# Optimization experiments

Measured on AMD Instinct MI355X. Metric: run time of the kernel, lower is better.

## Reference

```python
import jax, jax.numpy as jnp
import numpy as np

N = 50000      # nodes
E = 600000     # edges (avg degree 12)
D_IN = 16      # node_input_size
D = 128        # hidden_size
H = 4          # num_heads
DH = D // H
L = 4          # message_passing_num
D_FF = 512     # 4*hidden FFN expansion
D_OUT = 3      # output_size


def setup_inputs() -> dict:
    key = jax.random.key(0)
    ks = iter(jax.random.split(key, 32))
    def w(shape, fan_in):
        return jax.random.normal(next(ks), shape, jnp.float32) / np.float32(np.sqrt(fan_in))
    return {
        "features": jax.random.normal(next(ks), (N, D_IN), jnp.float32),
        "senders": jax.random.randint(next(ks), (E,), 0, N),
        "receivers": jax.random.randint(next(ks), (E,), 0, N),
        "enc_w1": w((D_IN, D), D_IN), "enc_b1": jnp.zeros((D,), jnp.float32),
        "enc_w2": w((D, D), D),       "enc_b2": jnp.zeros((D,), jnp.float32),
        "wq": w((L, D, D), D), "wk": w((L, D, D), D),
        "wv": w((L, D, D), D), "wo": w((L, D, D), D),
        "ln1_s": jnp.ones((L, D), jnp.float32), "ln1_b": jnp.zeros((L, D), jnp.float32),
        "ffn_w1": w((L, D, D_FF), D), "ffn_b1": jnp.zeros((L, D_FF), jnp.float32),
        "ffn_w2": w((L, D_FF, D), D_FF), "ffn_b2": jnp.zeros((L, D), jnp.float32),
        "ln2_s": jnp.ones((L, D), jnp.float32), "ln2_b": jnp.zeros((L, D), jnp.float32),
        "dec_w1": w((D, D_OUT), D), "dec_b1": jnp.zeros((D_OUT,), jnp.float32),
        "dec_w2": w((D_OUT, D_OUT), D_OUT), "dec_b2": jnp.zeros((D_OUT,), jnp.float32),
    }


def _ln(x, s, b):
    mu = x.mean(-1, keepdims=True)
    var = ((x - mu) ** 2).mean(-1, keepdims=True)
    return (x - mu) * jax.lax.rsqrt(var + 1e-5) * s + b


def _graph_mha(x, senders, receivers, wq, wk, wv, wo):
    # Adjacency-masked attention done sparsely over the edge list
    # (equivalent to softmax over the BCOO adjacency pattern).
    n = x.shape[0]
    q = (x @ wq).reshape(n, H, DH)
    k = (x @ wk).reshape(n, H, DH)
    v = (x @ wv).reshape(n, H, DH)
    scores = (q[receivers] * k[senders]).sum(-1) / np.float32(np.sqrt(DH))  # [E,H]
    m = jax.ops.segment_max(scores, receivers, num_segments=n)             # [N,H]
    m = jnp.where(jnp.isfinite(m), m, 0.0)
    a = jnp.exp(scores - m[receivers])                                      # [E,H]
    denom = jax.ops.segment_sum(a, receivers, num_segments=n)              # [N,H]
    msg = jax.ops.segment_sum(a[:, :, None] * v[senders], receivers, num_segments=n)  # [N,H,DH]
    out = (msg / (denom[:, :, None] + 1e-9)).reshape(n, D)
    return out @ wo


def reference(features, senders, receivers,
              enc_w1, enc_b1, enc_w2, enc_b2,
              wq, wk, wv, wo, ln1_s, ln1_b,
              ffn_w1, ffn_b1, ffn_w2, ffn_b2, ln2_s, ln2_b,
              dec_w1, dec_b1, dec_w2, dec_b2):
    # encode
    x = jnp.maximum(features @ enc_w1 + enc_b1, 0.0) @ enc_w2 + enc_b2     # [N,D]
    # process: L pre-LN sparse-attention transformer blocks
    for l in range(L):
        h = _ln(x, ln1_s[l], ln1_b[l])
        x = x + _graph_mha(h, senders, receivers, wq[l], wk[l], wv[l], wo[l])
        h = _ln(x, ln2_s[l], ln2_b[l])
        x = x + jnp.maximum(h @ ffn_w1[l] + ffn_b1[l], 0.0) @ ffn_w2[l] + ffn_b2[l]
    # decode
    return jnp.maximum(x @ dec_w1 + dec_b1, 0.0) @ dec_w2 + dec_b2         # [N,D_OUT]
```

## Files before the change

kernel.cpp:

```cpp
#include <hip/hip_runtime.h>
#include <hip/hip_bf16.h>
#include <math.h>

#define D     128
#define NHEAD 4
#define DH    32
#define DFF   512
#define DIN   16
#define MAXDEG 64
#define TN    16

typedef __attribute__((ext_vector_type(8))) short bf16x8;
typedef __attribute__((ext_vector_type(4))) float f32x4;
typedef __hip_bfloat16 bf16;

#define QSCALE_L2E 0.2550348838f

#define BMQ 128

#define WAITV(N) asm volatile("s_waitcnt vmcnt(" #N ")" ::: "memory")
#define WAITLGKM asm volatile("s_waitcnt lgkmcnt(0)" ::: "memory")
#define FENCE()  asm volatile("" ::: "memory")
#define BAR() do { FENCE(); __builtin_amdgcn_s_barrier(); FENCE(); } while (0)

__device__ __forceinline__ void gll16(const bf16* g, bf16* l) {
    __builtin_amdgcn_global_load_lds((__attribute__((address_space(1))) void*)g,
                                     (__attribute__((address_space(3))) void*)l,
                                     16, 0, 0);
}

__device__ __forceinline__ ushort bfbits(float f) {
    __hip_bfloat16 b = __float2bfloat16(f);
    return *(ushort*)&b;
}

__global__ void k_fill(const int* __restrict__ recv, const int* __restrict__ senders,
                       int* __restrict__ deg, int* __restrict__ eid, int E) {
    int e = blockIdx.x * blockDim.x + threadIdx.x;
    if (e >= E) return;
    int r = recv[e];
    int pos = atomicAdd(&deg[r], 1);
    if (pos < MAXDEG) eid[r * MAXDEG + pos] = senders[e];
}

__global__ void k_wt(const float* __restrict__ wq, const float* __restrict__ wk,
                     const float* __restrict__ wv, const float* __restrict__ wo,
                     const float* __restrict__ w1, const float* __restrict__ w2,
                     const float* __restrict__ encw2,
                     bf16* __restrict__ wqkvT, bf16* __restrict__ woT,
                     bf16* __restrict__ w1T, bf16* __restrict__ w2T,
                     bf16* __restrict__ encw2T, int* __restrict__ deg,
                     int* __restrict__ eid, int N) {
    int r = blockIdx.y;
    if (r == 25) {
        int tot = N + N * MAXDEG;
        for (int i = blockIdx.x * blockDim.x + threadIdx.x; i < tot;
             i += 256 * 256) {
            if (i < N) deg[i] = 0;
            else eid[i - N] = 0;
        }
        return;
    }
    const float* src; bf16* dst; int K, Nout;
    if (r < 12) {
        int l = r / 3, sel = r % 3;
        src = (sel == 0 ? wq : sel == 1 ? wk : wv) + (size_t)l * D * D;
        dst = wqkvT + (size_t)l * 3 * D * D + (size_t)sel * D * D;
        K = D; Nout = D;
    } else if (r < 16) {
        int l = r - 12;
        src = wo + (size_t)l * D * D; dst = woT + (size_t)l * D * D; K = D; Nout = D;
    } else if (r < 20) {
        int l = r - 16;
        src = w1 + (size_t)l * D * DFF; dst = w1T + (size_t)l * D * DFF; K = D; Nout = DFF;
    } else if (r < 24) {
        int l = r - 20;
        src = w2 + (size_t)l * DFF * D; dst = w2T + (size_t)l * DFF * D; K = DFF; Nout = D;
    } else {
        src = encw2; dst = encw2T; K = D; Nout = D;
    }
    int total = K * Nout;
    int i = blockIdx.x * blockDim.x + threadIdx.x;
    if (i >= total) return;
    int k = i / Nout, j = i % Nout;
    dst[(size_t)j * K + k] = __float2bfloat16(src[i]);
}

__device__ __forceinline__ void load_afrag(const bf16* A, int arow, int quad,
                                           int N, bf16x8* afr) {
    const bf16* ab = A + (size_t)arow * D + quad * 8;
#pragma unroll
    for (int i = 0; i < 4; i++) {
        uint4 v = make_uint4(0u, 0u, 0u, 0u);
        if (arow < N) v = *(const uint4*)(ab + i * 32);
        afr[i] = *(bf16x8*)&v;
    }
}

__device__ __forceinline__ void stage_full256(bf16* lb, const bf16* src,
                                              int wave, int lane) {
#pragma unroll
    for (int k = 0; k < 8; k++) {
        int gidx = (wave * 8 + k) * 64 + lane;
        int r = gidx >> 4, gL = gidx & 15;
        gll16(src + (size_t)r * 128 + ((gL ^ (r & 15)) * 8),
              lb + (size_t)(wave * 8 + k) * 512);
    }
}

__device__ __forceinline__ void stage_full512(bf16* lb, const bf16* src,
                                              int wave, int lane) {
#pragma unroll
    for (int k = 0; k < 4; k++) {
        int gidx = (wave * 4 + k) * 64 + lane;
        int r = gidx >> 4, gL = gidx & 15;
        gll16(src + (size_t)r * 128 + ((gL ^ (r & 15)) * 8),
              lb + (size_t)(wave * 4 + k) * 512);
    }
}

__device__ __forceinline__ void stage_q(bf16* lb, const bf16* src, int rs,
                                        int wave, int lane) {
#pragma unroll
    for (int k = 0; k < 2; k++) {
        int gidx = (wave * 2 + k) * 64 + lane;
        int r = gidx >> 2, gL = gidx & 3;
        gll16(src + (size_t)r * rs + ((gL ^ ((r >> 1) & 3)) * 8),
              lb + (size_t)(wave * 2 + k) * 512);
    }
}

__device__ __forceinline__ void mfma_tile(const bf16* Wb, const bf16x8* afr,
                                          f32x4* acc, int l16, int quad) {
#pragma unroll
    for (int i = 0; i < 4; i++)
#pragma unroll
        for (int j = 0; j < 8; j++) {
            const bf16* wp = Wb + (size_t)(j * 16 + l16) * 128
                              + (size_t)((((i * 4 + quad)) ^ l16) * 8);
            acc[j] = __builtin_amdgcn_mfma_f32_16x16x32_bf16(afr[i], *(const bf16x8*)wp,
                                                             acc[j], 0, 0, 0);
        }
}

template<int OP>
__global__ __launch_bounds__(256) void k_gemm(
        const bf16* __restrict__ A, const bf16* __restrict__ Bt,
        const float* __restrict__ bias,
        const float* __restrict__ lns, const float* __restrict__ lnb,
        float* x, bf16* outB, int N) {
    __shared__ alignas(16) bf16 Wsm[128 * 128];
    int m0 = blockIdx.x * 64;
    int t = threadIdx.x;
    int wave = t >> 6, lane = t & 63;
    int quad = lane >> 4, l16 = lane & 15;
    int wm = wave * 16;

    bf16x8 afr[4];
    load_afrag(A, m0 + wm + l16, quad, N, afr);
    FENCE();
    stage_full256(Wsm, Bt, wave, lane);
    WAITV(0); BAR();

    int rowb = m0 + wm + quad * 4;
    float xv[8][4];
    if (OP == 2) {
#pragma unroll
        for (int j = 0; j < 8; j++)
#pragma unroll
            for (int r = 0; r < 4; r++) {
                int gr = rowb + r;
                xv[j][r] = (gr < N) ? x[(size_t)gr * D + j * 16 + l16] : 0.f;
            }
    }

    f32x4 acc[8];
#pragma unroll
    for (int j = 0; j < 8; j++) acc[j] = (f32x4){0.f, 0.f, 0.f, 0.f};
    mfma_tile(Wsm, afr, acc, l16, quad);

    float bv[8];
    if (OP == 5) {
#pragma unroll
        for (int j = 0; j < 8; j++) bv[j] = bias[j * 16 + l16];
    }
#pragma unroll
    for (int j = 0; j < 8; j++) {
#pragma unroll
        for (int r = 0; r < 4; r++) {
            int gr = rowb + r;
            if (gr >= N) continue;
            float val = acc[j][r];
            if (OP == 5) val += bv[j];
            if (OP == 2) val += xv[j][r];
            acc[j][r] = val;
        }
    }
    float lsv[8], lbv[8];
#pragma unroll
    for (int j = 0; j < 8; j++) {
        lsv[j] = lns[j * 16 + l16];
        lbv[j] = lnb[j * 16 + l16];
    }
#pragma unroll
    for (int r = 0; r < 4; r++) {
        float s1 = 0.f, s2 = 0.f;
#pragma unroll
        for (int j = 0; j < 8; j++) {
            float v = acc[j][r];
            s1 += v; s2 += v * v;
        }
        s1 += __shfl_xor(s1, 1, 64);  s2 += __shfl_xor(s2, 1, 64);
        s1 += __shfl_xor(s1, 2, 64);  s2 += __shfl_xor(s2, 2, 64);
        s1 += __shfl_xor(s1, 4, 64);  s2 += __shfl_xor(s2, 4, 64);
        s1 += __shfl_xor(s1, 8, 64);  s2 += __shfl_xor(s2, 8, 64);
        float mu = s1 * (1.f / 128.f);
        float var = s2 * (1.f / 128.f) - mu * mu;
        float rinv = rsqrtf(fmaxf(var, 0.f) + 1e-5f);
        int gr = rowb + r;
        if (gr >= N) continue;
#pragma unroll
        for (int j = 0; j < 8; j++) {
            int col = j * 16 + l16;
            float v = acc[j][r];
            x[(size_t)gr * D + col] = v;
            outB[(size_t)gr * D + col] =
                __float2bfloat16((v - mu) * rinv * lsv[j] + lbv[j]);
        }
    }
}

__global__ __launch_bounds__(512, 2) void k_qkv(
        const bf16* __restrict__ hb, const bf16* __restrict__ wqkvT,
        bf16* __restrict__ qb, bf16* __restrict__ kvb, int N) {
    __shared__ alignas(16) bf16 Wbuf[2][128 * 128];
    int m0 = blockIdx.x * BMQ;
    int t = threadIdx.x;
    int wave = t >> 6, lane = t & 63;
    int quad = lane >> 4, l16 = lane & 15;
    int wm = wave * 16;

    bf16x8 afr[4];
    load_afrag(hb, m0 + wm + l16, quad, N, afr);
    FENCE();
    stage_full512(Wbuf[0], wqkvT + (size_t)D * D, wave, lane);
    FENCE();
    stage_full512(Wbuf[1], wqkvT + (size_t)2 * D * D, wave, lane);
    FENCE();

    int rowb = m0 + wm + quad * 4;
    f32x4 ak[8], acc[8];
#pragma unroll
    for (int j = 0; j < 8; j++) ak[j] = (f32x4){0.f, 0.f, 0.f, 0.f};

    WAITV(4); BAR();
    __builtin_amdgcn_s_setprio(1);
    mfma_tile(Wbuf[0], afr, ak, l16, quad);
    __builtin_amdgcn_s_setprio(0);
    BAR();
    stage_full512(Wbuf[0], wqkvT, wave, lane);
    FENCE();
#pragma unroll
    for (int j = 0; j < 8; j++) acc[j] = (f32x4){0.f, 0.f, 0.f, 0.f};
    WAITV(4); BAR();
    __builtin_amdgcn_s_setprio(1);
    mfma_tile(Wbuf[1], afr, acc, l16, quad);
    __builtin_amdgcn_s_setprio(0);

#pragma unroll
    for (int j = 0; j < 8; j++) {
        int col = j * 16 + l16;
#pragma unroll
        for (int r = 0; r < 4; r++) {
            int gr = rowb + r;
            if (gr >= N) continue;
            uint kv = (uint)bfbits(ak[j][r]) | ((uint)bfbits(acc[j][r]) << 16);
            *(uint*)&kvb[((size_t)gr * D + col) * 2] = kv;
        }
    }
    FENCE();
    if (m0 + BMQ <= N) { WAITV(32); } else { WAITV(0); }
    BAR();
#pragma unroll
    for (int j = 0; j < 8; j++) acc[j] = (f32x4){0.f, 0.f, 0.f, 0.f};
    __builtin_amdgcn_s_setprio(1);
    mfma_tile(Wbuf[0], afr, acc, l16, quad);
    __builtin_amdgcn_s_setprio(0);
#pragma unroll
    for (int j = 0; j < 8; j++) {
        int col = j * 16 + l16;
#pragma unroll
        for (int r = 0; r < 4; r++) {
            int gr = rowb + r;
            if (gr >= N) continue;
            qb[(size_t)gr * D + col] = __float2bfloat16(acc[j][r] * QSCALE_L2E);
        }
    }
}

__device__ __forceinline__ void stage_ffn_q(int ts, const bf16* w1T,
                                            const bf16* w2T, bf16* Wb3,
                                            int wave, int lane) {
    int c = ts >> 3, p = ts & 7;
    const bf16* src; int rs;
    if (p < 4) { src = w1T + (size_t)(c * 128) * 128 + p * 32;       rs = 128; }
    else       { src = w2T + (size_t)(c * 128) + (p - 4) * 32;       rs = DFF; }
    stage_q(Wb3 + (size_t)(ts % 3) * (32 * 128), src, rs, wave, lane);
}

template<int MODE>
__global__ __launch_bounds__(256) void k_ffn(
        const bf16* __restrict__ hb, const bf16* __restrict__ w1T,
        const float* __restrict__ b1,
        const bf16* __restrict__ w2T, const float* __restrict__ b2,
        const float* __restrict__ lns, const float* __restrict__ lnb,
        const float* __restrict__ dw1, const float* __restrict__ db1,
        const float* __restrict__ dw2, const float* __restrict__ db2,
        float* x, bf16* outB, float* out, int N) {
    __shared__ alignas(16) bf16 Wb3[3][32 * 128];
    __shared__ alignas(16) bf16 Hsm[64 * 128];
    int m0 = blockIdx.x * 64;
    int t = threadIdx.x;
    int wave = t >> 6, lane = t & 63;
    int quad = lane >> 4, l16 = lane & 15;
    int wm = wave * 16;
    int rowb = m0 + wm + quad * 4;

    float b1pre[4][8];
#pragma unroll
    for (int c2 = 0; c2 < 4; c2++)
#pragma unroll
        for (int j = 0; j < 8; j++) b1pre[c2][j] = b1[c2 * 128 + j * 16 + l16];

    bf16x8 afr[4];
    load_afrag(hb, m0 + wm + l16, quad, N, afr);
    FENCE();
    stage_ffn_q(0, w1T, w2T, &Wb3[0][0], wave, lane);
    FENCE();
    stage_ffn_q(1, w1T, w2T, &Wb3[0][0], wave, lane);
    FENCE();

    f32x4 acc2[8], accP[8];
#pragma unroll
    for (int j = 0; j < 8; j++) acc2[j] = (f32x4){0.f, 0.f, 0.f, 0.f};
    float xv[8][4];

    int wswz = (quad ^ ((l16 >> 1) & 3)) * 8;

#pragma unroll
    for (int s = 0; s < 32; s++) {
        BAR();
        if (s + 2 < 32) {
            stage_ffn_q(s + 2, w1T, w2T, &Wb3[0][0], wave, lane);
            FENCE();
        }
        if (s < 30) { WAITV(4); } else if (s == 30) { WAITV(2); } else { WAITV(0); }
        BAR();
        const bf16* Wb = &Wb3[0][0] + (size_t)(s % 3) * (32 * 128);
        int c = s >> 3, p = s & 7;
        if (s == 31) {
#pragma unroll
            for (int j = 0; j < 8; j++)
#pragma unroll
                for (int r = 0; r < 4; r++) {
                    int gr = rowb + r;
                    xv[j][r] = (gr < N) ? x[(size_t)gr * D + j * 16 + l16] : 0.f;
                }
        }
        if (p < 4) {
            if (p == 0) {
#pragma unroll
                for (int j = 0; j < 8; j++) accP[j] = (f32x4){0.f, 0.f, 0.f, 0.f};
            }
            __builtin_amdgcn_s_setprio(1);
#pragma unroll
            for (int j = 0; j < 8; j++) {
                const bf16* wp = Wb + (size_t)(j * 16 + l16) * 32 + wswz;
                accP[j] = __builtin_amdgcn_mfma_f32_16x16x32_bf16(
                    afr[p], *(const bf16x8*)wp, accP[j], 0, 0, 0);
            }
            __builtin_amdgcn_s_setprio(0);
            if (p == 3) {
                int rw = wm + quad * 4;
#pragma unroll
                for (int j = 0; j < 8; j++) {
                    int gb = j * 2 + (l16 >> 3), ce = l16 & 7;
#pragma unroll
                    for (int r = 0; r < 4; r++) {
                        int row = rw + r;
                        Hsm[(size_t)row * 128 + (size_t)((gb ^ (row & 15)) * 8) + ce] =
                            __float2bfloat16(fmaxf(accP[j][r] + b1pre[c][j], 0.f));
                    }
                }
                WAITLGKM;
            }
        } else {
            int kq = p - 4;
            bf16x8 af2 = *(const bf16x8*)(Hsm + (size_t)(wm + l16) * 128
                              + (size_t)(((kq * 4 + quad) ^ l16) * 8));
            __builtin_amdgcn_s_setprio(1);
#pragma unroll
            for (int j = 0; j < 8; j++) {
                const bf16* wp = Wb + (size_t)(j * 16 + l16) * 32 + wswz;
                acc2[j] = __builtin_amdgcn_mfma_f32_16x16x32_bf16(
                    af2, *(const bf16x8*)wp, acc2[j], 0, 0, 0);
            }
            __builtin_amdgcn_s_setprio(0);
        }
    }

    float bv[8];
#pragma unroll
    for (int j = 0; j < 8; j++) bv[j] = b2[j * 16 + l16];
#pragma unroll
    for (int j = 0; j < 8; j++) {
#pragma unroll
        for (int r = 0; r < 4; r++) {
            int gr = rowb + r;
            if (gr >= N) continue;
            acc2[j][r] += bv[j] + xv[j][r];
        }
    }
    if (MODE == 1) {
        float dw[8][3];
#pragma unroll
        for (int j = 0; j < 8; j++) {
            int col = j * 16 + l16;
#pragma unroll
            for (int cc3 = 0; cc3 < 3; cc3++) dw[j][cc3] = dw1[col * 3 + cc3];
        }
#pragma unroll
        for (int r = 0; r < 4; r++) {
            float s0 = 0.f, s1 = 0.f, s2 = 0.f;
#pragma unroll
            for (int j = 0; j < 8; j++) {
                float v = acc2[j][r];
                s0 += v * dw[j][0]; s1 += v * dw[j][1]; s2 += v * dw[j][2];
            }
            s0 += __shfl_xor(s0, 1, 64); s1 += __shfl_xor(s1, 1, 64); s2 += __shfl_xor(s2, 1, 64);
            s0 += __shfl_xor(s0, 2, 64); s1 += __shfl_xor(s1, 2, 64); s2 += __shfl_xor(s2, 2, 64);
            s0 += __shfl_xor(s0, 4, 64); s1 += __shfl_xor(s1, 4, 64); s2 += __shfl_xor(s2, 4, 64);
            s0 += __shfl_xor(s0, 8, 64); s1 += __shfl_xor(s1, 8, 64); s2 += __shfl_xor(s2, 8, 64);
            int gr = rowb + r;
            if (l16 == 0 && gr < N) {
                float t0 = fmaxf(s0 + db1[0], 0.f);
                float t1 = fmaxf(s1 + db1[1], 0.f);
                float t2 = fmaxf(s2 + db1[2], 0.f);
#pragma unroll
                for (int o = 0; o < 3; o++)
                    out[(size_t)gr * 3 + o] =
                        t0 * dw2[0 * 3 + o] + t1 * dw2[1 * 3 + o] + t2 * dw2[2 * 3 + o] + db2[o];
            }
        }
        return;
    }
    float lsv[8], lbv[8];
#pragma unroll
    for (int j = 0; j < 8; j++) {
        lsv[j] = lns[j * 16 + l16];
        lbv[j] = lnb[j * 16 + l16];
    }
#pragma unroll
    for (int r = 0; r < 4; r++) {
        float s1 = 0.f, s2 = 0.f;
#pragma unroll
        for (int j = 0; j < 8; j++) {
            float v = acc2[j][r];
            s1 += v; s2 += v * v;
        }
        s1 += __shfl_xor(s1, 1, 64);  s2 += __shfl_xor(s2, 1, 64);
        s1 += __shfl_xor(s1, 2, 64);  s2 += __shfl_xor(s2, 2, 64);
        s1 += __shfl_xor(s1, 4, 64);  s2 += __shfl_xor(s2, 4, 64);
        s1 += __shfl_xor(s1, 8, 64);  s2 += __shfl_xor(s2, 8, 64);
        float mu = s1 * (1.f / 128.f);
        float var = s2 * (1.f / 128.f) - mu * mu;
        float rinv = rsqrtf(fmaxf(var, 0.f) + 1e-5f);
        int gr = rowb + r;
        if (gr >= N) continue;
#pragma unroll
        for (int j = 0; j < 8; j++) {
            int col = j * 16 + l16;
            float v = acc2[j][r];
            x[(size_t)gr * D + col] = v;
            outB[(size_t)gr * D + col] = __float2bfloat16((v - mu) * rinv * lsv[j] + lbv[j]);
        }
    }
}

__global__ void k_enc1(const float* __restrict__ feat,
                       const float* __restrict__ w1, const float* __restrict__ b1,
                       bf16* __restrict__ hb, int N) {
    __shared__ float fsh[TN][DIN];
    int n0 = blockIdx.x * TN;
    int j = threadIdx.x;
    int nvalid = min(TN, N - n0);
    for (int idx = j; idx < TN * DIN; idx += 128) {
        int n = idx / DIN, i = idx % DIN;
        fsh[n][i] = (n < nvalid) ? feat[(n0 + n) * DIN + i] : 0.f;
    }
    __syncthreads();
    float bb = b1[j];
#pragma unroll
    for (int n = 0; n < TN; n++) {
        float a = bb;
#pragma unroll
        for (int i = 0; i < DIN; i++) a += fsh[n][i] * w1[i * D + j];
        if (n < nvalid) hb[(size_t)(n0 + n) * D + j] = __float2bfloat16(fmaxf(a, 0.f));
    }
}

__device__ __forceinline__ void attn_edge(uint4 w, bool v, float4 qv,
                                          float& l, float& a0, float& a1,
                                          float& a2, float& a3) {
    float k0 = __uint_as_float(w.x << 16), v0 = __uint_as_float(w.x & 0xFFFF0000u);
    float k1 = __uint_as_float(w.y << 16), v1 = __uint_as_float(w.y & 0xFFFF0000u);
    float k2 = __uint_as_float(w.z << 16), v2 = __uint_as_float(w.z & 0xFFFF0000u);
    float k3 = __uint_as_float(w.w << 16), v3 = __uint_as_float(w.w & 0xFFFF0000u);
    float p = qv.x * k0 + qv.y * k1 + qv.z * k2 + qv.w * k3;
    p += __shfl_xor(p, 1, 64);
    p += __shfl_xor(p, 2, 64);
    p += __shfl_xor(p, 4, 64);
    float e = v ? exp2f(p) : 0.f;
    l += e;
    a0 += e * v0; a1 += e * v1; a2 += e * v2; a3 += e * v3;
}

__device__ __forceinline__ float4 unpackq(uint2 qw) {
    float4 qv;
    qv.x = __uint_as_float(qw.x << 16);
    qv.y = __uint_as_float(qw.x & 0xFFFF0000u);
    qv.z = __uint_as_float(qw.y << 16);
    qv.w = __uint_as_float(qw.y & 0xFFFF0000u);
    return qv;
}

__global__ __launch_bounds__(256) void k_attn(
        const bf16* __restrict__ qb, const uint* __restrict__ kvb,
        const int* __restrict__ deg, const int* __restrict__ eid,
        bf16* __restrict__ out, int N) {
    int wave = threadIdx.x >> 6, lane = threadIdx.x & 63;
    int g = lane & 7, h = (lane >> 3) & 3, slot = lane >> 5;
    int d0 = h * 32 + g * 4;
    int rbase = blockIdx.x * 16 + wave * 4;
    if (rbase >= N) return;
    const uint* kvbase = kvb + d0;

    int ssN[8];
    {
        const int* row = eid + (size_t)rbase * MAXDEG;
#pragma unroll
        for (int u = 0; u < 8; u++) ssN[u] = row[u * 2 + slot];
    }
    int cntN = min(deg[rbase], MAXDEG);
    float4 qvN = unpackq(*(const uint2*)(qb + (size_t)rbase * D + d0));

#pragma unroll
    for (int i = 0; i < 4; i++) {
        int r = rbase + i;
        if (r >= N) return;
        int cnt = cntN; float4 qv = qvN;
        uint4 w[8];
#pragma unroll
        for (int u = 0; u < 8; u++)
            w[u] = *(const uint4*)(kvbase + (size_t)ssN[u] * D);
        int rn = r + 1;
        if (i < 3 && rn < N) {
            const int* rowN = eid + (size_t)rn * MAXDEG;
#pragma unroll
            for (int u = 0; u < 8; u++) ssN[u] = rowN[u * 2 + slot];
            cntN = min(deg[rn], MAXDEG);
            qvN = unpackq(*(const uint2*)(qb + (size_t)rn * D + d0));
        }
        float l = 0.f, a0 = 0.f, a1 = 0.f, a2 = 0.f, a3 = 0.f;
#pragma unroll
        for (int u = 0; u < 8; u++)
            attn_edge(w[u], (u * 2 + slot) < cnt, qv, l, a0, a1, a2, a3);
        for (int base = 16; base < cnt; base += 16) {
            const int* row = eid + (size_t)r * MAXDEG;
            int ss[8]; bool vv[8];
#pragma unroll
            for (int u = 0; u < 8; u++) {
                int e = base + u * 2 + slot;
                vv[u] = e < cnt;
                ss[u] = row[e];
            }
            uint4 w2_[8];
#pragma unroll
            for (int u = 0; u < 8; u++)
                w2_[u] = *(const uint4*)(kvbase + (size_t)ss[u] * D);
#pragma unroll
            for (int u = 0; u < 8; u++)
                attn_edge(w2_[u], vv[u], qv, l, a0, a1, a2, a3);
        }
        l  += __shfl_xor(l, 32, 64);
        a0 += __shfl_xor(a0, 32, 64);
        a1 += __shfl_xor(a1, 32, 64);
        a2 += __shfl_xor(a2, 32, 64);
        a3 += __shfl_xor(a3, 32, 64);
        if (lane < 32) {
            float inv = 1.f / (l + 1e-9f);
            bf16 o[4];
            o[0] = __float2bfloat16(a0 * inv);
            o[1] = __float2bfloat16(a1 * inv);
            o[2] = __float2bfloat16(a2 * inv);
            o[3] = __float2bfloat16(a3 * inv);
            *(uint2*)(out + (size_t)r * D + d0) = *(uint2*)o;
        }
    }
}

extern "C" void kernel_launch(void* const* d_in, const int* in_sizes, int n_in,
                              void* d_out, int out_size, void* d_ws, size_t ws_size,
                              hipStream_t stream) {
    const float* feat    = (const float*)d_in[0];
    const int*   senders = (const int*)d_in[1];
    const int*   recv    = (const int*)d_in[2];
    const float* enc_w1  = (const float*)d_in[3];
    const float* enc_b1  = (const float*)d_in[4];
    const float* enc_w2  = (const float*)d_in[5];
    const float* enc_b2  = (const float*)d_in[6];
    const float* wq      = (const float*)d_in[7];
    const float* wk      = (const float*)d_in[8];
    const float* wv      = (const float*)d_in[9];
    const float* wo      = (const float*)d_in[10];
    const float* ln1_s   = (const float*)d_in[11];
    const float* ln1_b   = (const float*)d_in[12];
    const float* ffn_w1  = (const float*)d_in[13];
    const float* ffn_b1  = (const float*)d_in[14];
    const float* ffn_w2  = (const float*)d_in[15];
    const float* ffn_b2  = (const float*)d_in[16];
    const float* ln2_s   = (const float*)d_in[17];
    const float* ln2_b   = (const float*)d_in[18];
    const float* dec_w1  = (const float*)d_in[19];
    const float* dec_b1  = (const float*)d_in[20];
    const float* dec_w2  = (const float*)d_in[21];
    const float* dec_b2  = (const float*)d_in[22];

    int N = in_sizes[0] / DIN;
    int E = in_sizes[1];

    char* p = (char*)d_ws;
    float* x   = (float*)p;  p += (size_t)N * D * 4;
    bf16*  qb  = (bf16*)p;   p += (size_t)N * D * 2;
    bf16*  kvb = (bf16*)p;   p += (size_t)N * D * 2 * 2;
    bf16*  hb  = (bf16*)p;   p += (size_t)N * D * 2;
    int* deg   = (int*)p;    p += (size_t)N * 4;
    int* eid   = (int*)p;    p += (size_t)N * MAXDEG * 4;
    bf16* wqkvT  = (bf16*)p; p += (size_t)4 * 3 * D * D * 2;
    bf16* woT    = (bf16*)p; p += (size_t)4 * D * D * 2;
    bf16* w1T    = (bf16*)p; p += (size_t)4 * D * DFF * 2;
    bf16* w2T    = (bf16*)p; p += (size_t)4 * DFF * D * 2;
    bf16* encw2T = (bf16*)p; p += (size_t)D * D * 2;

    int gm64 = (N + 63) / 64;
    int gmQ  = (N + BMQ - 1) / BMQ;

    k_wt<<<dim3(256, 26), 256, 0, stream>>>(wq, wk, wv, wo, ffn_w1, ffn_w2, enc_w2,
                                            wqkvT, woT, w1T, w2T, encw2T, deg, eid, N);
    k_fill<<<(E + 255) / 256, 256, 0, stream>>>(recv, senders, deg, eid, E);
    k_enc1<<<(N + TN - 1) / TN, 128, 0, stream>>>(feat, enc_w1, enc_b1, hb, N);
    k_gemm<5><<<gm64, 256, 0, stream>>>(hb, encw2T, enc_b2, ln1_s, ln1_b, x, hb, N);

    for (int l = 0; l < 4; l++) {
        k_qkv<<<gmQ, 512, 0, stream>>>(hb, wqkvT + (size_t)l * 3 * D * D, qb, kvb, N);
        k_attn<<<(N + 15) / 16, 256, 0, stream>>>(qb, (const uint*)kvb, deg, eid, hb, N);
        k_gemm<2><<<gm64, 256, 0, stream>>>(hb, woT + (size_t)l * D * D,
                                            nullptr, ln2_s + l * D, ln2_b + l * D,
                                            x, hb, N);
        if (l < 3)
            k_ffn<0><<<gm64, 256, 0, stream>>>(hb, w1T + (size_t)l * D * DFF,
                                               ffn_b1 + l * DFF,
                                               w2T + (size_t)l * DFF * D, ffn_b2 + l * D,
                                               ln1_s + (l + 1) * D, ln1_b + (l + 1) * D,
                                               nullptr, nullptr, nullptr, nullptr,
                                               x, hb, nullptr, N);
        else
            k_ffn<1><<<gm64, 256, 0, stream>>>(hb, w1T + (size_t)l * D * DFF,
                                               ffn_b1 + l * DFF,
                                               w2T + (size_t)l * DFF * D, ffn_b2 + l * D,
                                               nullptr, nullptr,
                                               dec_w1, dec_b1, dec_w2, dec_b2,
                                               x, nullptr, (float*)d_out, N);
    }
}
```

Before: 644.3 us.

## Drop eid zero-fill and simplify attention to one row per wave

The setup kernel no longer zeroes the N×MAXDEG neighbour table and clears only the degree array. The attention kernel now guards neighbour-index loads with the edge count, so the stale table entries are never read. The attention kernel also goes from four rows per wave, with software prefetch of the next row's indices and query, to one row per wave with a uniform loop. This removes a large memset (about 12.8 MB) at the cost of losing cross-row prefetch overlap in attention, and launches four times as many blocks.

```diff
diff --git a/kernel.cpp b/kernel.cpp
--- a/kernel.cpp
+++ b/kernel.cpp
@@ -16,7 +16,7 @@
 
 #define QSCALE_L2E 0.2550348838f
 
-#define BMQ 128
+#define BM 128
 
 #define WAITV(N) asm volatile("s_waitcnt vmcnt(" #N ")" ::: "memory")
 #define WAITLGKM asm volatile("s_waitcnt lgkmcnt(0)" ::: "memory")
@@ -49,16 +49,11 @@
                      const float* __restrict__ encw2,
                      bf16* __restrict__ wqkvT, bf16* __restrict__ woT,
                      bf16* __restrict__ w1T, bf16* __restrict__ w2T,
-                     bf16* __restrict__ encw2T, int* __restrict__ deg,
-                     int* __restrict__ eid, int N) {
+                     bf16* __restrict__ encw2T, int* __restrict__ deg, int N) {
     int r = blockIdx.y;
     if (r == 25) {
-        int tot = N + N * MAXDEG;
-        for (int i = blockIdx.x * blockDim.x + threadIdx.x; i < tot;
-             i += 256 * 256) {
-            if (i < N) deg[i] = 0;
-            else eid[i - N] = 0;
-        }
+        int i = blockIdx.x * blockDim.x + threadIdx.x;
+        if (i < N) deg[i] = 0;
         return;
     }
     const float* src; bf16* dst; int K, Nout;
@@ -234,7 +229,7 @@
         const bf16* __restrict__ hb, const bf16* __restrict__ wqkvT,
         bf16* __restrict__ qb, bf16* __restrict__ kvb, int N) {
     __shared__ alignas(16) bf16 Wbuf[2][128 * 128];
-    int m0 = blockIdx.x * BMQ;
+    int m0 = blockIdx.x * BM;
     int t = threadIdx.x;
     int wave = t >> 6, lane = t & 63;
     int quad = lane >> 4, l16 = lane & 15;
@@ -279,7 +274,7 @@
         }
     }
     FENCE();
-    if (m0 + BMQ <= N) { WAITV(32); } else { WAITV(0); }
+    if (m0 + BM <= N) { WAITV(32); } else { WAITV(0); }
     BAR();
 #pragma unroll
     for (int j = 0; j < 8; j++) acc[j] = (f32x4){0.f, 0.f, 0.f, 0.f};
@@ -525,87 +520,57 @@
     a0 += e * v0; a1 += e * v1; a2 += e * v2; a3 += e * v3;
 }
 
-__device__ __forceinline__ float4 unpackq(uint2 qw) {
+__global__ __launch_bounds__(256) void k_attn(
+        const bf16* __restrict__ qb, const uint* __restrict__ kvb,
+        const int* __restrict__ deg, const int* __restrict__ eid,
+        bf16* __restrict__ out, int N) {
+    int wave = threadIdx.x >> 6, lane = threadIdx.x & 63;
+    int r = blockIdx.x * 4 + wave;
+    if (r >= N) return;
+    int g = lane & 7;
+    int h = (lane >> 3) & 3;
+    int slot = lane >> 5;
+    int d0 = h * 32 + g * 4;
+    uint2 qw = *(const uint2*)(qb + (size_t)r * D + d0);
     float4 qv;
     qv.x = __uint_as_float(qw.x << 16);
     qv.y = __uint_as_float(qw.x & 0xFFFF0000u);
     qv.z = __uint_as_float(qw.y << 16);
     qv.w = __uint_as_float(qw.y & 0xFFFF0000u);
-    return qv;
-}
-
-__global__ __launch_bounds__(256) void k_attn(
-        const bf16* __restrict__ qb, const uint* __restrict__ kvb,
-        const int* __restrict__ deg, const int* __restrict__ eid,
-        bf16* __restrict__ out, int N) {
-    int wave = threadIdx.x >> 6, lane = threadIdx.x & 63;
-    int g = lane & 7, h = (lane >> 3) & 3, slot = lane >> 5;
-    int d0 = h * 32 + g * 4;
-    int rbase = blockIdx.x * 16 + wave * 4;
-    if (rbase >= N) return;
+    int cnt = min(deg[r], MAXDEG);
+    const int* row = eid + (size_t)r * MAXDEG;
     const uint* kvbase = kvb + d0;
-
-    int ssN[8];
-    {
-        const int* row = eid + (size_t)rbase * MAXDEG;
-#pragma unroll
-        for (int u = 0; u < 8; u++) ssN[u] = row[u * 2 + slot];
-    }
-    int cntN = min(deg[rbase], MAXDEG);
-    float4 qvN = unpackq(*(const uint2*)(qb + (size_t)rbase * D + d0));
-
-#pragma unroll
-    for (int i = 0; i < 4; i++) {
-        int r = rbase + i;
-        if (r >= N) return;
-        int cnt = cntN; float4 qv = qvN;
+    float l = 0.f, a0 = 0.f, a1 = 0.f, a2 = 0.f, a3 = 0.f;
+    for (int base = 0; base < cnt; base += 16) {
+        int ss[8];
+        bool vv[8];
+#pragma unroll
+        for (int u = 0; u < 8; u++) {
+            int e = base + u * 2 + slot;
+            vv[u] = e < cnt;
+            ss[u] = vv[u] ? row[e] : 0;
+        }
         uint4 w[8];
 #pragma unroll
         for (int u = 0; u < 8; u++)
-            w[u] = *(const uint4*)(kvbase + (size_t)ssN[u] * D);
-        int rn = r + 1;
-        if (i < 3 && rn < N) {
-            const int* rowN = eid + (size_t)rn * MAXDEG;
-#pragma unroll
-            for (int u = 0; u < 8; u++) ssN[u] = rowN[u * 2 + slot];
-            cntN = min(deg[rn], MAXDEG);
-            qvN = unpackq(*(const uint2*)(qb + (size_t)rn * D + d0));
-        }
-        float l = 0.f, a0 = 0.f, a1 = 0.f, a2 = 0.f, a3 = 0.f;
+            w[u] = *(const uint4*)(kvbase + (size_t)ss[u] * D);
 #pragma unroll
         for (int u = 0; u < 8; u++)
-            attn_edge(w[u], (u * 2 + slot) < cnt, qv, l, a0, a1, a2, a3);
-        for (int base = 16; base < cnt; base += 16) {
-            const int* row = eid + (size_t)r * MAXDEG;
-            int ss[8]; bool vv[8];
-#pragma unroll
-            for (int u = 0; u < 8; u++) {
-                int e = base + u * 2 + slot;
-                vv[u] = e < cnt;
-                ss[u] = row[e];
-            }
-            uint4 w2_[8];
-#pragma unroll
-            for (int u = 0; u < 8; u++)
-                w2_[u] = *(const uint4*)(kvbase + (size_t)ss[u] * D);
-#pragma unroll
-            for (int u = 0; u < 8; u++)
-                attn_edge(w2_[u], vv[u], qv, l, a0, a1, a2, a3);
-        }
-        l  += __shfl_xor(l, 32, 64);
-        a0 += __shfl_xor(a0, 32, 64);
-        a1 += __shfl_xor(a1, 32, 64);
-        a2 += __shfl_xor(a2, 32, 64);
-        a3 += __shfl_xor(a3, 32, 64);
-        if (lane < 32) {
-            float inv = 1.f / (l + 1e-9f);
-            bf16 o[4];
-            o[0] = __float2bfloat16(a0 * inv);
-            o[1] = __float2bfloat16(a1 * inv);
-            o[2] = __float2bfloat16(a2 * inv);
-            o[3] = __float2bfloat16(a3 * inv);
-            *(uint2*)(out + (size_t)r * D + d0) = *(uint2*)o;
-        }
+            attn_edge(w[u], vv[u], qv, l, a0, a1, a2, a3);
+    }
+    l  += __shfl_xor(l, 32, 64);
+    a0 += __shfl_xor(a0, 32, 64);
+    a1 += __shfl_xor(a1, 32, 64);
+    a2 += __shfl_xor(a2, 32, 64);
+    a3 += __shfl_xor(a3, 32, 64);
+    if (lane < 32) {
+        float inv = 1.f / (l + 1e-9f);
+        bf16 o[4];
+        o[0] = __float2bfloat16(a0 * inv);
+        o[1] = __float2bfloat16(a1 * inv);
+        o[2] = __float2bfloat16(a2 * inv);
+        o[3] = __float2bfloat16(a3 * inv);
+        *(uint2*)(out + (size_t)r * D + d0) = *(uint2*)o;
     }
 }
 
@@ -653,17 +618,17 @@
     bf16* encw2T = (bf16*)p; p += (size_t)D * D * 2;
 
     int gm64 = (N + 63) / 64;
-    int gmQ  = (N + BMQ - 1) / BMQ;
+    int gmQ  = (N + BM - 1) / BM;
 
     k_wt<<<dim3(256, 26), 256, 0, stream>>>(wq, wk, wv, wo, ffn_w1, ffn_w2, enc_w2,
-                                            wqkvT, woT, w1T, w2T, encw2T, deg, eid, N);
+                                            wqkvT, woT, w1T, w2T, encw2T, deg, N);
     k_fill<<<(E + 255) / 256, 256, 0, stream>>>(recv, senders, deg, eid, E);
     k_enc1<<<(N + TN - 1) / TN, 128, 0, stream>>>(feat, enc_w1, enc_b1, hb, N);
     k_gemm<5><<<gm64, 256, 0, stream>>>(hb, encw2T, enc_b2, ln1_s, ln1_b, x, hb, N);
 
     for (int l = 0; l < 4; l++) {
         k_qkv<<<gmQ, 512, 0, stream>>>(hb, wqkvT + (size_t)l * 3 * D * D, qb, kvb, N);
-        k_attn<<<(N + 15) / 16, 256, 0, stream>>>(qb, (const uint*)kvb, deg, eid, hb, N);
+        k_attn<<<(N + 3) / 4, 256, 0, stream>>>(qb, (const uint*)kvb, deg, eid, hb, N);
         k_gemm<2><<<gm64, 256, 0, stream>>>(hb, woT + (size_t)l * D * D,
                                             nullptr, ln2_s + l * D, ln2_b + l * D,
                                             x, hb, N);
```

Measured after the change: 641.7 us. Within noise of the previous version (-0.4%).
